# Performance work log

Hardware: AMD Instinct MI355X
Metric: run time of the kernel (lower is better)

The kernel has to match this reference:

```python
import jax, jax.numpy as jnp
import numpy as np
import math

B = 1048576          # number of query points
D = 3                # input_dim
L = 16               # num_levels
C = 2                # level_dim (features per level)
H = 16               # base_resolution
S = 1.0              # log2(per_level_scale)
LOG2_T = 19
MAX_PARAMS = 2 ** LOG2_T
HASH_ENTRIES = 524288
ALIGN = False        # align_corners
PRIMES = (1, 2654435761, 805459861)  # tcnn spatial hash primes


def _make_offsets():
    offs = [0]
    off = 0
    for l in range(L):
        res = int(np.ceil(H * (2.0 ** (S * l))))
        n = min(MAX_PARAMS, (res if ALIGN else res + 1) ** D)
        n = int(np.ceil(n / 8) * 8)
        off += n
        offs.append(off)
    return offs

OFFSETS = _make_offsets()
N_TABLE = OFFSETS[-1]  # 7131240
# 2^D corner offsets, corner i has bit d = (i >> d) & 1
_CORNERS = np.array([[(i >> d) & 1 for d in range(D)] for i in range(2 ** D)], dtype=np.uint32)


def _grid_encode(x01, table):
    """x01: [B, D] coords in [0, 1]; table: [N_TABLE, C]. Returns [B, L*C]."""
    corners_u = jnp.asarray(_CORNERS)                  # [8, D] uint32
    corners_b = jnp.asarray(_CORNERS.astype(bool))     # [8, D]
    outs = []
    for l in range(L):
        scale = (2.0 ** (S * l)) * H - 1.0
        res = int(math.ceil(scale)) + 1
        side = res if ALIGN else res + 1               # per-dim stride base
        hm = OFFSETS[l + 1] - OFFSETS[l]               # hashmap size of this level
        pos = x01 * jnp.float32(scale) + jnp.float32(0.0 if ALIGN else 0.5)
        pg = jnp.floor(pos)
        frac = pos - pg                                # [B, D]
        cg = pg.astype(jnp.uint32)[:, None, :] + corners_u[None]  # [B, 8, D]
        # trilinear weights: prod of frac (corner bit 1) or 1-frac (bit 0)
        w = jnp.prod(jnp.where(corners_b[None], frac[:, None, :], 1.0 - frac[:, None, :]), axis=-1)  # [B, 8]
        if side ** D <= hm:
            # dense (non-hashed) stride indexing
            strides = jnp.asarray(np.array([side ** d for d in range(D)], dtype=np.uint32))
            idx = jnp.sum(cg * strides[None, None, :], axis=-1, dtype=jnp.uint32) % jnp.uint32(hm)
        else:
            # spatial hash: xor of coord * prime, wrapping uint32 arithmetic
            h = cg[..., 0] * jnp.uint32(PRIMES[0])
            for d in range(1, D):
                h = h ^ (cg[..., d] * jnp.uint32(PRIMES[d]))
            idx = h % jnp.uint32(hm)
        feats = table[(idx + jnp.uint32(OFFSETS[l])).astype(jnp.int32)]   # [B, 8, C] gather
        outs.append(jnp.sum(w[..., None] * feats, axis=1))                # [B, C]
    # matches outputs.permute(1,0,2).reshape(B, L*C): level features concatenated per point
    return jnp.concatenate(outs, axis=-1)


def setup_inputs():
    key = jax.random.key(0)
    k1, k2, k3 = jax.random.split(key, 3)
    inputs = jax.random.uniform(k1, (B, D), dtype=jnp.float32, minval=-1.0, maxval=1.0)
    ext_embeddings = jax.random.uniform(k2, (HASH_ENTRIES, C), dtype=jnp.float32, minval=-1e-4, maxval=1e-4)
    own_embeddings = jax.random.uniform(k3, (N_TABLE - HASH_ENTRIES, C), dtype=jnp.float32, minval=-1e-4, maxval=1e-4)
    return {"inputs": inputs, "ext_embeddings": ext_embeddings, "own_embeddings": own_embeddings}


def reference(inputs, ext_embeddings, own_embeddings):
    bound = 1.0
    table = jnp.concatenate([ext_embeddings, own_embeddings], axis=0)  # [N_TABLE, C]
    x01 = (inputs + bound) / (2.0 * bound)
    return _grid_encode(x01, table)
```

## Files before the change

### kernel.cpp

```cpp
#include <hip/hip_runtime.h>
#include <hip/hip_cooperative_groups.h>
#include <stdint.h>

namespace cg = cooperative_groups;


constexpr uint32_t OFF[16] = {
    0u, 4920u, 40864u, 315496u, 839784u, 1364072u, 1888360u, 2412648u,
    2936936u, 3461224u, 3985512u, 4509800u, 5034088u, 5558376u, 6082664u, 6606952u
};

#define HASH_ENTRIES 524288u
#define HASH_MASK    (HASH_ENTRIES - 1u)
#define P1 2654435761u
#define P2 805459861u

typedef float floatx2 __attribute__((ext_vector_type(2)));
typedef float floatx4 __attribute__((ext_vector_type(4)));

template<int L>
__device__ __forceinline__ void do_level(
    float x01, float y01, float z01,
    const float2* __restrict__ ext, const float2* __restrict__ own,
    float* __restrict__ ws, int B, int p)
{
    constexpr float scale = (float)((16u << L) - 1u);
    const float px = x01 * scale + 0.5f;
    const float py = y01 * scale + 0.5f;
    const float pz = z01 * scale + 0.5f;
    const float fxf = floorf(px), fyf = floorf(py), fzf = floorf(pz);
    const float tx = px - fxf, ty = py - fyf, tz = pz - fzf;
    const uint32_t x0 = (uint32_t)(int)fxf;
    const uint32_t y0 = (uint32_t)(int)fyf;
    const uint32_t z0 = (uint32_t)(int)fzf;

    float2 f[8];
    if constexpr (L < 3) {
        constexpr uint32_t side = (16u << L) + 1u;
        constexpr uint32_t s2 = side * side;
        const uint32_t base = OFF[L] + x0 + y0 * side + z0 * s2;
#pragma unroll
        for (int i = 0; i < 8; ++i) {
            f[i] = ext[base + (uint32_t)(i & 1)
                           + (uint32_t)((i >> 1) & 1) * side
                           + (uint32_t)((i >> 2) & 1) * s2];
        }
    } else {
        const uint32_t hx0 = x0,       hx1 = x0 + 1u;
        const uint32_t hy0 = y0 * P1,  hy1 = (y0 + 1u) * P1;
        const uint32_t hz0 = z0 * P2,  hz1 = (z0 + 1u) * P2;
#pragma unroll
        for (int i = 0; i < 8; ++i) {
            const uint32_t gi = (((i & 1) ? hx1 : hx0) ^
                                 ((i & 2) ? hy1 : hy0) ^
                                 ((i & 4) ? hz1 : hz0)) & HASH_MASK;
            if constexpr (L == 3) {
                const uint32_t gg = gi + OFF[3];
                const float2* q = (gg < HASH_ENTRIES)
                                    ? (ext + gg)
                                    : (own + (gg - HASH_ENTRIES));
                f[i] = *q;
            } else {
                f[i] = own[(OFF[L] - HASH_ENTRIES) + gi];
            }
        }
    }

    float r0 = 0.0f, r1 = 0.0f;
#pragma unroll
    for (int i = 0; i < 8; ++i) {
        const float wi = ((i & 1) ? tx : 1.0f - tx)
                       * ((i & 2) ? ty : 1.0f - ty)
                       * ((i & 4) ? tz : 1.0f - tz);
        r0 += wi * f[i].x;
        r1 += wi * f[i].y;
    }
    floatx2 v = { r0, r1 };
    __builtin_nontemporal_store(v, (floatx2*)(ws + (size_t)L * 2 * B + 2 * p));
}

__global__ __launch_bounds__(256, 4) void coop_kernel(
    const float* __restrict__ xyz,
    const float2* __restrict__ ext,
    const float2* __restrict__ own,
    float* __restrict__ ws,
    float* __restrict__ out,
    int B)
{
    cg::grid_group grid = cg::this_grid();
    const int NT  = (int)(gridDim.x * 256u);
    const int tid = (int)(blockIdx.x * 256u + threadIdx.x);

    float cx[4], cy[4], cz[4];
#pragma unroll
    for (int i = 0; i < 4; ++i) {
        const int p = tid + i * NT;
        if (p < B) {
            cx[i] = (__builtin_nontemporal_load(&xyz[3 * p + 0]) + 1.0f) * 0.5f;
            cy[i] = (__builtin_nontemporal_load(&xyz[3 * p + 1]) + 1.0f) * 0.5f;
            cz[i] = (__builtin_nontemporal_load(&xyz[3 * p + 2]) + 1.0f) * 0.5f;
        } else {
            cx[i] = cy[i] = cz[i] = 0.0f;
        }
    }

#define LEVEL_STEP(L)                                                        \
    {                                                                        \
        _Pragma("unroll")                                                    \
        for (int i = 0; i < 4; ++i) {                                        \
            const int p = tid + i * NT;                                      \
            if (p < B) do_level<L>(cx[i], cy[i], cz[i], ext, own, ws, B, p); \
        }                                                                    \
        grid.sync();                                                         \
    }

    LEVEL_STEP(0)  LEVEL_STEP(1)  LEVEL_STEP(2)  LEVEL_STEP(3)
    LEVEL_STEP(4)  LEVEL_STEP(5)  LEVEL_STEP(6)  LEVEL_STEP(7)
    LEVEL_STEP(8)  LEVEL_STEP(9)  LEVEL_STEP(10) LEVEL_STEP(11)
    LEVEL_STEP(12) LEVEL_STEP(13) LEVEL_STEP(14) LEVEL_STEP(15)
#undef LEVEL_STEP

#pragma unroll
    for (int i = 0; i < 4; ++i) {
        const int p = tid + i * NT;
        if (p >= B) continue;
        float v[32];
#pragma unroll
        for (int l = 0; l < 16; ++l) {
            floatx2 t = *(const floatx2*)(ws + (size_t)l * 2 * B + 2 * p);
            v[2 * l + 0] = t.x;
            v[2 * l + 1] = t.y;
        }
        floatx4* o4 = (floatx4*)(out + (size_t)p * 32);
#pragma unroll
        for (int k = 0; k < 8; ++k) {
            floatx4 q = { v[4 * k + 0], v[4 * k + 1],
                          v[4 * k + 2], v[4 * k + 3] };
            o4[k] = q;
        }
    }
}

template<int L, bool DIRECT>
__global__ __launch_bounds__(256) void phase_kernel(
    const float* __restrict__ xyz,
    const float2* __restrict__ ext,
    const float2* __restrict__ own,
    float* __restrict__ dst,
    int B)
{
    const int b = blockIdx.x * 256 + threadIdx.x;
    if (b >= B) return;
    const float x01 = (__builtin_nontemporal_load(&xyz[3 * b + 0]) + 1.0f) * 0.5f;
    const float y01 = (__builtin_nontemporal_load(&xyz[3 * b + 1]) + 1.0f) * 0.5f;
    const float z01 = (__builtin_nontemporal_load(&xyz[3 * b + 2]) + 1.0f) * 0.5f;
    if constexpr (DIRECT) {
        constexpr float scale = (float)((16u << L) - 1u);
        const float px = x01 * scale + 0.5f;
        const float py = y01 * scale + 0.5f;
        const float pz = z01 * scale + 0.5f;
        const float fxf = floorf(px), fyf = floorf(py), fzf = floorf(pz);
        const float tx = px - fxf, ty = py - fyf, tz = pz - fzf;
        const uint32_t x0 = (uint32_t)(int)fxf;
        const uint32_t y0 = (uint32_t)(int)fyf;
        const uint32_t z0 = (uint32_t)(int)fzf;
        float2 f[8];
        if constexpr (L < 3) {
            constexpr uint32_t side = (16u << L) + 1u;
            constexpr uint32_t s2 = side * side;
            const uint32_t base = OFF[L] + x0 + y0 * side + z0 * s2;
#pragma unroll
            for (int i = 0; i < 8; ++i)
                f[i] = ext[base + (uint32_t)(i & 1)
                               + (uint32_t)((i >> 1) & 1) * side
                               + (uint32_t)((i >> 2) & 1) * s2];
        } else {
            const uint32_t hx0 = x0,       hx1 = x0 + 1u;
            const uint32_t hy0 = y0 * P1,  hy1 = (y0 + 1u) * P1;
            const uint32_t hz0 = z0 * P2,  hz1 = (z0 + 1u) * P2;
#pragma unroll
            for (int i = 0; i < 8; ++i) {
                const uint32_t gi = (((i & 1) ? hx1 : hx0) ^
                                     ((i & 2) ? hy1 : hy0) ^
                                     ((i & 4) ? hz1 : hz0)) & HASH_MASK;
                if constexpr (L == 3) {
                    const uint32_t gg = gi + OFF[3];
                    const float2* q = (gg < HASH_ENTRIES)
                                        ? (ext + gg)
                                        : (own + (gg - HASH_ENTRIES));
                    f[i] = *q;
                } else {
                    f[i] = own[(OFF[L] - HASH_ENTRIES) + gi];
                }
            }
        }
        float r0 = 0.0f, r1 = 0.0f;
#pragma unroll
        for (int i = 0; i < 8; ++i) {
            const float wi = ((i & 1) ? tx : 1.0f - tx)
                           * ((i & 2) ? ty : 1.0f - ty)
                           * ((i & 4) ? tz : 1.0f - tz);
            r0 += wi * f[i].x;
            r1 += wi * f[i].y;
        }
        floatx2 v = { r0, r1 };
        *(floatx2*)(dst + (size_t)b * 32 + 2 * L) = v;
    } else {
        do_level<L>(x01, y01, z01, ext, own, dst, B, b);
    }
}

__global__ __launch_bounds__(256) void transpose_kernel(
    const float* __restrict__ ws, float* __restrict__ out, int B)
{
    const int b = blockIdx.x * 256 + threadIdx.x;
    if (b >= B) return;
    float v[32];
#pragma unroll
    for (int l = 0; l < 16; ++l) {
        floatx2 t = *(const floatx2*)(ws + (size_t)l * 2 * B + 2 * b);
        v[2 * l + 0] = t.x;
        v[2 * l + 1] = t.y;
    }
    floatx4* o4 = (floatx4*)(out + (size_t)b * 32);
#pragma unroll
    for (int k = 0; k < 8; ++k) {
        floatx4 q = { v[4 * k + 0], v[4 * k + 1], v[4 * k + 2], v[4 * k + 3] };
        o4[k] = q;
    }
}

template<bool DIRECT>
static inline void launch_phases(const float* xyz, const float2* ext,
                                 const float2* own, float* dst, int B,
                                 int grid, hipStream_t stream) {
    phase_kernel< 0, DIRECT><<<grid, 256, 0, stream>>>(xyz, ext, own, dst, B);
    phase_kernel< 1, DIRECT><<<grid, 256, 0, stream>>>(xyz, ext, own, dst, B);
    phase_kernel< 2, DIRECT><<<grid, 256, 0, stream>>>(xyz, ext, own, dst, B);
    phase_kernel< 3, DIRECT><<<grid, 256, 0, stream>>>(xyz, ext, own, dst, B);
    phase_kernel< 4, DIRECT><<<grid, 256, 0, stream>>>(xyz, ext, own, dst, B);
    phase_kernel< 5, DIRECT><<<grid, 256, 0, stream>>>(xyz, ext, own, dst, B);
    phase_kernel< 6, DIRECT><<<grid, 256, 0, stream>>>(xyz, ext, own, dst, B);
    phase_kernel< 7, DIRECT><<<grid, 256, 0, stream>>>(xyz, ext, own, dst, B);
    phase_kernel< 8, DIRECT><<<grid, 256, 0, stream>>>(xyz, ext, own, dst, B);
    phase_kernel< 9, DIRECT><<<grid, 256, 0, stream>>>(xyz, ext, own, dst, B);
    phase_kernel<10, DIRECT><<<grid, 256, 0, stream>>>(xyz, ext, own, dst, B);
    phase_kernel<11, DIRECT><<<grid, 256, 0, stream>>>(xyz, ext, own, dst, B);
    phase_kernel<12, DIRECT><<<grid, 256, 0, stream>>>(xyz, ext, own, dst, B);
    phase_kernel<13, DIRECT><<<grid, 256, 0, stream>>>(xyz, ext, own, dst, B);
    phase_kernel<14, DIRECT><<<grid, 256, 0, stream>>>(xyz, ext, own, dst, B);
    phase_kernel<15, DIRECT><<<grid, 256, 0, stream>>>(xyz, ext, own, dst, B);
}

extern "C" void kernel_launch(void* const* d_in, const int* in_sizes, int n_in,
                              void* d_out, int out_size, void* d_ws, size_t ws_size,
                              hipStream_t stream) {
    const float*  xyz = (const float*)d_in[0];
    const float2* ext = (const float2*)d_in[1];
    const float2* own = (const float2*)d_in[2];
    float* out = (float*)d_out;
    const int B = in_sizes[0] / 3;
    const int grid = (B + 255) / 256;
    const size_t need = (size_t)B * 32 * sizeof(float);

    int dev = 0;
    hipGetDevice(&dev);
    int cus = 0;
    hipDeviceGetAttribute(&cus, hipDeviceAttributeMultiprocessorCount, dev);
    int occ = 0;
    hipOccupancyMaxActiveBlocksPerMultiprocessor(&occ, coop_kernel, 256, 0);
    const int gridNeeded = (B + 4 * 256 - 1) / (4 * 256);

    if (ws_size >= need && occ > 0 && (long)occ * cus >= gridNeeded) {
        float* ws = (float*)d_ws;
        int Bv = B;
        void* args[6];
        args[0] = (void*)&xyz; args[1] = (void*)&ext; args[2] = (void*)&own;
        args[3] = (void*)&ws;  args[4] = (void*)&out; args[5] = (void*)&Bv;
        hipLaunchCooperativeKernel((const void*)coop_kernel,
                                   dim3(gridNeeded), dim3(256), args, 0, stream);
    } else if (ws_size >= need) {
        float* ws = (float*)d_ws;
        launch_phases<false>(xyz, ext, own, ws, B, grid, stream);
        transpose_kernel<<<grid, 256, 0, stream>>>(ws, out, B);
    } else {
        launch_phases<true>(xyz, ext, own, out, B, grid, stream);
    }
}
```

Baseline: 662.8 us.

## Batch hash gathers across points, fuse dense levels into final pass, double occupancy

The cooperative kernel now handles 2 points per thread instead of 4 and raises launch bounds to 8 blocks per CU. Each hash level computes all corner indices for both points first, then issues all 16 gathers, so more loads are in flight. The three dense levels, whose tables are small and cache-resident, are computed directly in the final output pass, which removes three grid syncs and shrinks the workspace to 26 floats per point. The risks are higher register pressure from the batched gathers under the tighter register budget, and a larger grid that must still fit co-resident for the cooperative launch.

```diff
diff --git a/kernel.cpp b/kernel.cpp
--- a/kernel.cpp
+++ b/kernel.cpp
@@ -14,16 +14,83 @@
 #define HASH_MASK    (HASH_ENTRIES - 1u)
 #define P1 2654435761u
 #define P2 805459861u
+#define PPT 2
 
 typedef float floatx2 __attribute__((ext_vector_type(2)));
 typedef float floatx4 __attribute__((ext_vector_type(4)));
 
 template<int L>
-__device__ __forceinline__ void do_level(
-    float x01, float y01, float z01,
+__device__ __forceinline__ void hash_phase(
+    const float* cx, const float* cy, const float* cz,
     const float2* __restrict__ ext, const float2* __restrict__ own,
-    float* __restrict__ ws, int B, int p)
+    float* __restrict__ ws, int B, int tid, int NT)
 {
+    static_assert(L >= 3, "hash levels only");
+    uint32_t gi[PPT][8];
+    float txa[PPT], tya[PPT], tza[PPT];
+#pragma unroll
+    for (int i = 0; i < PPT; ++i) {
+        constexpr float scale = (float)((16u << L) - 1u);
+        const float px = cx[i] * scale + 0.5f;
+        const float py = cy[i] * scale + 0.5f;
+        const float pz = cz[i] * scale + 0.5f;
+        const float fxf = floorf(px), fyf = floorf(py), fzf = floorf(pz);
+        txa[i] = px - fxf; tya[i] = py - fyf; tza[i] = pz - fzf;
+        const uint32_t x0 = (uint32_t)(int)fxf;
+        const uint32_t y0 = (uint32_t)(int)fyf;
+        const uint32_t z0 = (uint32_t)(int)fzf;
+        const uint32_t hx0 = x0,       hx1 = x0 + 1u;
+        const uint32_t hy0 = y0 * P1,  hy1 = (y0 + 1u) * P1;
+        const uint32_t hz0 = z0 * P2,  hz1 = (z0 + 1u) * P2;
+#pragma unroll
+        for (int c = 0; c < 8; ++c) {
+            gi[i][c] = (((c & 1) ? hx1 : hx0) ^
+                        ((c & 2) ? hy1 : hy0) ^
+                        ((c & 4) ? hz1 : hz0)) & HASH_MASK;
+        }
+    }
+
+    float2 f[PPT][8];
+#pragma unroll
+    for (int i = 0; i < PPT; ++i) {
+#pragma unroll
+        for (int c = 0; c < 8; ++c) {
+            if constexpr (L == 3) {
+                const uint32_t gg = gi[i][c] + OFF[3];
+                const float2* q = (gg < HASH_ENTRIES)
+                                    ? (ext + gg)
+                                    : (own + (gg - HASH_ENTRIES));
+                f[i][c] = *q;
+            } else {
+                f[i][c] = own[(OFF[L] - HASH_ENTRIES) + gi[i][c]];
+            }
+        }
+    }
+
+#pragma unroll
+    for (int i = 0; i < PPT; ++i) {
+        const int p = tid + i * NT;
+        if (p >= B) continue;
+        float r0 = 0.0f, r1 = 0.0f;
+#pragma unroll
+        for (int c = 0; c < 8; ++c) {
+            const float wi = ((c & 1) ? txa[i] : 1.0f - txa[i])
+                           * ((c & 2) ? tya[i] : 1.0f - tya[i])
+                           * ((c & 4) ? tza[i] : 1.0f - tza[i]);
+            r0 += wi * f[i][c].x;
+            r1 += wi * f[i][c].y;
+        }
+        floatx2 v = { r0, r1 };
+        __builtin_nontemporal_store(v,
+            (floatx2*)(ws + (size_t)(L - 3) * 2 * B + 2 * p));
+    }
+}
+
+template<int L>
+__device__ __forceinline__ float2 dense_level(
+    float x01, float y01, float z01, const float2* __restrict__ ext)
+{
+    static_assert(L < 3, "dense levels only");
     constexpr float scale = (float)((16u << L) - 1u);
     const float px = x01 * scale + 0.5f;
     const float py = y01 * scale + 0.5f;
@@ -33,18 +100,125 @@
     const uint32_t x0 = (uint32_t)(int)fxf;
     const uint32_t y0 = (uint32_t)(int)fyf;
     const uint32_t z0 = (uint32_t)(int)fzf;
-
+    constexpr uint32_t side = (16u << L) + 1u;
+    constexpr uint32_t s2 = side * side;
+    const uint32_t base = OFF[L] + x0 + y0 * side + z0 * s2;
+    float r0 = 0.0f, r1 = 0.0f;
+#pragma unroll
+    for (int c = 0; c < 8; ++c) {
+        const float2 f = ext[base + (uint32_t)(c & 1)
+                                  + (uint32_t)((c >> 1) & 1) * side
+                                  + (uint32_t)((c >> 2) & 1) * s2];
+        const float wi = ((c & 1) ? tx : 1.0f - tx)
+                       * ((c & 2) ? ty : 1.0f - ty)
+                       * ((c & 4) ? tz : 1.0f - tz);
+        r0 += wi * f.x;
+        r1 += wi * f.y;
+    }
+    return make_float2(r0, r1);
+}
+
+__global__ __launch_bounds__(256, 8) void coop_kernel(
+    const float* __restrict__ xyz,
+    const float2* __restrict__ ext,
+    const float2* __restrict__ own,
+    float* __restrict__ ws,
+    float* __restrict__ out,
+    int B)
+{
+    cg::grid_group grid = cg::this_grid();
+    const int NT  = (int)(gridDim.x * 256u);
+    const int tid = (int)(blockIdx.x * 256u + threadIdx.x);
+
+    float cx[PPT], cy[PPT], cz[PPT];
+#pragma unroll
+    for (int i = 0; i < PPT; ++i) {
+        const int p = tid + i * NT;
+        if (p < B) {
+            cx[i] = (__builtin_nontemporal_load(&xyz[3 * p + 0]) + 1.0f) * 0.5f;
+            cy[i] = (__builtin_nontemporal_load(&xyz[3 * p + 1]) + 1.0f) * 0.5f;
+            cz[i] = (__builtin_nontemporal_load(&xyz[3 * p + 2]) + 1.0f) * 0.5f;
+        } else {
+            cx[i] = cy[i] = cz[i] = 0.0f;
+        }
+    }
+
+#define HP(L) hash_phase<L>(cx, cy, cz, ext, own, ws, B, tid, NT)
+    HP(3);  grid.sync();
+    HP(4);  grid.sync();
+    HP(5);  grid.sync();
+    HP(6);  grid.sync();
+    HP(7);  grid.sync();
+    HP(8);  grid.sync();
+    HP(9);  grid.sync();
+    HP(10); grid.sync();
+    HP(11); grid.sync();
+    HP(12); grid.sync();
+    HP(13); grid.sync();
+    HP(14); grid.sync();
+    HP(15);
+#undef HP
+
+#pragma unroll
+    for (int i = 0; i < PPT; ++i) {
+        const int p = tid + i * NT;
+        if (p >= B) continue;
+        float v[32];
+        const float2 d0 = dense_level<0>(cx[i], cy[i], cz[i], ext);
+        const float2 d1 = dense_level<1>(cx[i], cy[i], cz[i], ext);
+        const float2 d2 = dense_level<2>(cx[i], cy[i], cz[i], ext);
+        v[0] = d0.x; v[1] = d0.y;
+        v[2] = d1.x; v[3] = d1.y;
+        v[4] = d2.x; v[5] = d2.y;
+#pragma unroll
+        for (int l = 3; l < 16; ++l) {
+            floatx2 t = __builtin_nontemporal_load(
+                (const floatx2*)(ws + (size_t)(l - 3) * 2 * B + 2 * p));
+            v[2 * l + 0] = t.x;
+            v[2 * l + 1] = t.y;
+        }
+        floatx4* o4 = (floatx4*)(out + (size_t)p * 32);
+#pragma unroll
+        for (int k = 0; k < 8; ++k) {
+            floatx4 q = { v[4 * k + 0], v[4 * k + 1],
+                          v[4 * k + 2], v[4 * k + 3] };
+            o4[k] = q;
+        }
+    }
+}
+
+template<int L>
+__global__ __launch_bounds__(256) void phase_kernel(
+    const float* __restrict__ xyz,
+    const float2* __restrict__ ext,
+    const float2* __restrict__ own,
+    float* __restrict__ dst,
+    int B)
+{
+    const int b = blockIdx.x * 256 + threadIdx.x;
+    if (b >= B) return;
+    const float x01 = (__builtin_nontemporal_load(&xyz[3 * b + 0]) + 1.0f) * 0.5f;
+    const float y01 = (__builtin_nontemporal_load(&xyz[3 * b + 1]) + 1.0f) * 0.5f;
+    const float z01 = (__builtin_nontemporal_load(&xyz[3 * b + 2]) + 1.0f) * 0.5f;
+    constexpr float scale = (float)((16u << L) - 1u);
+    const float px = x01 * scale + 0.5f;
+    const float py = y01 * scale + 0.5f;
+    const float pz = z01 * scale + 0.5f;
+    const float fxf = floorf(px), fyf = floorf(py), fzf = floorf(pz);
+    const float tx = px - fxf, ty = py - fyf, tz = pz - fzf;
+    const uint32_t x0 = (uint32_t)(int)fxf;
+    const uint32_t y0 = (uint32_t)(int)fyf;
+    const uint32_t z0 = (uint32_t)(int)fzf;
     float2 f[8];
     if constexpr (L < 3) {
         constexpr uint32_t side = (16u << L) + 1u;
         constexpr uint32_t s2 = side * side;
         const uint32_t base = OFF[L] + x0 + y0 * side + z0 * s2;
 #pragma unroll
-        for (int i = 0; i < 8; ++i) {
+        for (int i = 0; i < 8; ++i)
             f[i] = ext[base + (uint32_t)(i & 1)
                            + (uint32_t)((i >> 1) & 1) * side
                            + (uint32_t)((i >> 2) & 1) * s2];
-        }
     } else {
         const uint32_t hx0 = x0,       hx1 = x0 + 1u;
         const uint32_t hy0 = y0 * P1,  hy1 = (y0 + 1u) * P1;
@@ -65,7 +239,6 @@
             }
         }
     }
-
     float r0 = 0.0f, r1 = 0.0f;
 #pragma unroll
     for (int i = 0; i < 8; ++i) {
@@ -76,180 +249,28 @@
         r1 += wi * f[i].y;
     }
     floatx2 v = { r0, r1 };
-    __builtin_nontemporal_store(v, (floatx2*)(ws + (size_t)L * 2 * B + 2 * p));
-}
-
-__global__ __launch_bounds__(256, 4) void coop_kernel(
-    const float* __restrict__ xyz,
-    const float2* __restrict__ ext,
-    const float2* __restrict__ own,
-    float* __restrict__ ws,
-    float* __restrict__ out,
-    int B)
-{
-    cg::grid_group grid = cg::this_grid();
-    const int NT  = (int)(gridDim.x * 256u);
-    const int tid = (int)(blockIdx.x * 256u + threadIdx.x);
-
-    float cx[4], cy[4], cz[4];
-#pragma unroll
-    for (int i = 0; i < 4; ++i) {
-        const int p = tid + i * NT;
-        if (p < B) {
-            cx[i] = (__builtin_nontemporal_load(&xyz[3 * p + 0]) + 1.0f) * 0.5f;
-            cy[i] = (__builtin_nontemporal_load(&xyz[3 * p + 1]) + 1.0f) * 0.5f;
-            cz[i] = (__builtin_nontemporal_load(&xyz[3 * p + 2]) + 1.0f) * 0.5f;
-        } else {
-            cx[i] = cy[i] = cz[i] = 0.0f;
-        }
-    }
-
-#define LEVEL_STEP(L)                                                        \
-    {                                                                        \
-        _Pragma("unroll")                                                    \
-        for (int i = 0; i < 4; ++i) {                                        \
-            const int p = tid + i * NT;                                      \
-            if (p < B) do_level<L>(cx[i], cy[i], cz[i], ext, own, ws, B, p); \
-        }                                                                    \
-        grid.sync();                                                         \
-    }
-
-    LEVEL_STEP(0)  LEVEL_STEP(1)  LEVEL_STEP(2)  LEVEL_STEP(3)
-    LEVEL_STEP(4)  LEVEL_STEP(5)  LEVEL_STEP(6)  LEVEL_STEP(7)
-    LEVEL_STEP(8)  LEVEL_STEP(9)  LEVEL_STEP(10) LEVEL_STEP(11)
-    LEVEL_STEP(12) LEVEL_STEP(13) LEVEL_STEP(14) LEVEL_STEP(15)
-#undef LEVEL_STEP
-
-#pragma unroll
-    for (int i = 0; i < 4; ++i) {
-        const int p = tid + i * NT;
-        if (p >= B) continue;
-        float v[32];
-#pragma unroll
-        for (int l = 0; l < 16; ++l) {
-            floatx2 t = *(const floatx2*)(ws + (size_t)l * 2 * B + 2 * p);
-            v[2 * l + 0] = t.x;
-            v[2 * l + 1] = t.y;
-        }
-        floatx4* o4 = (floatx4*)(out + (size_t)p * 32);
-#pragma unroll
-        for (int k = 0; k < 8; ++k) {
-            floatx4 q = { v[4 * k + 0], v[4 * k + 1],
-                          v[4 * k + 2], v[4 * k + 3] };
-            o4[k] = q;
-        }
-    }
-}
-
-template<int L, bool DIRECT>
-__global__ __launch_bounds__(256) void phase_kernel(
-    const float* __restrict__ xyz,
-    const float2* __restrict__ ext,
-    const float2* __restrict__ own,
-    float* __restrict__ dst,
-    int B)
-{
-    const int b = blockIdx.x * 256 + threadIdx.x;
-    if (b >= B) return;
-    const float x01 = (__builtin_nontemporal_load(&xyz[3 * b + 0]) + 1.0f) * 0.5f;
-    const float y01 = (__builtin_nontemporal_load(&xyz[3 * b + 1]) + 1.0f) * 0.5f;
-    const float z01 = (__builtin_nontemporal_load(&xyz[3 * b + 2]) + 1.0f) * 0.5f;
-    if constexpr (DIRECT) {
-        constexpr float scale = (float)((16u << L) - 1u);
-        const float px = x01 * scale + 0.5f;
-        const float py = y01 * scale + 0.5f;
-        const float pz = z01 * scale + 0.5f;
-        const float fxf = floorf(px), fyf = floorf(py), fzf = floorf(pz);
-        const float tx = px - fxf, ty = py - fyf, tz = pz - fzf;
-        const uint32_t x0 = (uint32_t)(int)fxf;
-        const uint32_t y0 = (uint32_t)(int)fyf;
-        const uint32_t z0 = (uint32_t)(int)fzf;
-        float2 f[8];
-        if constexpr (L < 3) {
-            constexpr uint32_t side = (16u << L) + 1u;
-            constexpr uint32_t s2 = side * side;
-            const uint32_t base = OFF[L] + x0 + y0 * side + z0 * s2;
-#pragma unroll
-            for (int i = 0; i < 8; ++i)
-                f[i] = ext[base + (uint32_t)(i & 1)
-                               + (uint32_t)((i >> 1) & 1) * side
-                               + (uint32_t)((i >> 2) & 1) * s2];
-        } else {
-            const uint32_t hx0 = x0,       hx1 = x0 + 1u;
-            const uint32_t hy0 = y0 * P1,  hy1 = (y0 + 1u) * P1;
-            const uint32_t hz0 = z0 * P2,  hz1 = (z0 + 1u) * P2;
-#pragma unroll
-            for (int i = 0; i < 8; ++i) {
-                const uint32_t gi = (((i & 1) ? hx1 : hx0) ^
-                                     ((i & 2) ? hy1 : hy0) ^
-                                     ((i & 4) ? hz1 : hz0)) & HASH_MASK;
-                if constexpr (L == 3) {
-                    const uint32_t gg = gi + OFF[3];
-                    const float2* q = (gg < HASH_ENTRIES)
-                                        ? (ext + gg)
-                                        : (own + (gg - HASH_ENTRIES));
-                    f[i] = *q;
-                } else {
-                    f[i] = own[(OFF[L] - HASH_ENTRIES) + gi];
-                }
-            }
-        }
-        float r0 = 0.0f, r1 = 0.0f;
-#pragma unroll
-        for (int i = 0; i < 8; ++i) {
-            const float wi = ((i & 1) ? tx : 1.0f - tx)
-                           * ((i & 2) ? ty : 1.0f - ty)
-                           * ((i & 4) ? tz : 1.0f - tz);
-            r0 += wi * f[i].x;
-            r1 += wi * f[i].y;
-        }
-        floatx2 v = { r0, r1 };
-        *(floatx2*)(dst + (size_t)b * 32 + 2 * L) = v;
-    } else {
-        do_level<L>(x01, y01, z01, ext, own, dst, B, b);
-    }
-}
-
-__global__ __launch_bounds__(256) void transpose_kernel(
-    const float* __restrict__ ws, float* __restrict__ out, int B)
-{
-    const int b = blockIdx.x * 256 + threadIdx.x;
-    if (b >= B) return;
-    float v[32];
-#pragma unroll
-    for (int l = 0; l < 16; ++l) {
-        floatx2 t = *(const floatx2*)(ws + (size_t)l * 2 * B + 2 * b);
-        v[2 * l + 0] = t.x;
-        v[2 * l + 1] = t.y;
-    }
-    floatx4* o4 = (floatx4*)(out + (size_t)b * 32);
-#pragma unroll
-    for (int k = 0; k < 8; ++k) {
-        floatx4 q = { v[4 * k + 0], v[4 * k + 1], v[4 * k + 2], v[4 * k + 3] };
-        o4[k] = q;
-    }
-}
-
-template<bool DIRECT>
-static inline void launch_phases(const float* xyz, const float2* ext,
-                                 const float2* own, float* dst, int B,
-                                 int grid, hipStream_t stream) {
-    phase_kernel< 0, DIRECT><<<grid, 256, 0, stream>>>(xyz, ext, own, dst, B);
-    phase_kernel< 1, DIRECT><<<grid, 256, 0, stream>>>(xyz, ext, own, dst, B);
-    phase_kernel< 2, DIRECT><<<grid, 256, 0, stream>>>(xyz, ext, own, dst, B);
-    phase_kernel< 3, DIRECT><<<grid, 256, 0, stream>>>(xyz, ext, own, dst, B);
-    phase_kernel< 4, DIRECT><<<grid, 256, 0, stream>>>(xyz, ext, own, dst, B);
-    phase_kernel< 5, DIRECT><<<grid, 256, 0, stream>>>(xyz, ext, own, dst, B);
-    phase_kernel< 6, DIRECT><<<grid, 256, 0, stream>>>(xyz, ext, own, dst, B);
-    phase_kernel< 7, DIRECT><<<grid, 256, 0, stream>>>(xyz, ext, own, dst, B);
-    phase_kernel< 8, DIRECT><<<grid, 256, 0, stream>>>(xyz, ext, own, dst, B);
-    phase_kernel< 9, DIRECT><<<grid, 256, 0, stream>>>(xyz, ext, own, dst, B);
-    phase_kernel<10, DIRECT><<<grid, 256, 0, stream>>>(xyz, ext, own, dst, B);
-    phase_kernel<11, DIRECT><<<grid, 256, 0, stream>>>(xyz, ext, own, dst, B);
-    phase_kernel<12, DIRECT><<<grid, 256, 0, stream>>>(xyz, ext, own, dst, B);
-    phase_kernel<13, DIRECT><<<grid, 256, 0, stream>>>(xyz, ext, own, dst, B);
-    phase_kernel<14, DIRECT><<<grid, 256, 0, stream>>>(xyz, ext, own, dst, B);
-    phase_kernel<15, DIRECT><<<grid, 256, 0, stream>>>(xyz, ext, own, dst, B);
+    *(floatx2*)(dst + (size_t)b * 32 + 2 * L) = v;
+}
+
+static inline void launch_fallback(const float* xyz, const float2* ext,
+                                   const float2* own, float* dst, int B,
+                                   int grid, hipStream_t stream) {
+    phase_kernel< 0><<<grid, 256, 0, stream>>>(xyz, ext, own, dst, B);
+    phase_kernel< 1><<<grid, 256, 0, stream>>>(xyz, ext, own, dst, B);
+    phase_kernel< 2><<<grid, 256, 0, stream>>>(xyz, ext, own, dst, B);
+    phase_kernel< 3><<<grid, 256, 0, stream>>>(xyz, ext, own, dst, B);
+    phase_kernel< 4><<<grid, 256, 0, stream>>>(xyz, ext, own, dst, B);
+    phase_kernel< 5><<<grid, 256, 0, stream>>>(xyz, ext, own, dst, B);
+    phase_kernel< 6><<<grid, 256, 0, stream>>>(xyz, ext, own, dst, B);
+    phase_kernel< 7><<<grid, 256, 0, stream>>>(xyz, ext, own, dst, B);
+    phase_kernel< 8><<<grid, 256, 0, stream>>>(xyz, ext, own, dst, B);
+    phase_kernel< 9><<<grid, 256, 0, stream>>>(xyz, ext, own, dst, B);
+    phase_kernel<10><<<grid, 256, 0, stream>>>(xyz, ext, own, dst, B);
+    phase_kernel<11><<<grid, 256, 0, stream>>>(xyz, ext, own, dst, B);
+    phase_kernel<12><<<grid, 256, 0, stream>>>(xyz, ext, own, dst, B);
+    phase_kernel<13><<<grid, 256, 0, stream>>>(xyz, ext, own, dst, B);
+    phase_kernel<14><<<grid, 256, 0, stream>>>(xyz, ext, own, dst, B);
+    phase_kernel<15><<<grid, 256, 0, stream>>>(xyz, ext, own, dst, B);
 }
 
 extern "C" void kernel_launch(void* const* d_in, const int* in_sizes, int n_in,
@@ -260,8 +281,7 @@
     const float2* own = (const float2*)d_in[2];
     float* out = (float*)d_out;
     const int B = in_sizes[0] / 3;
-    const int grid = (B + 255) / 256;
-    const size_t need = (size_t)B * 32 * sizeof(float);
+    const size_t need = (size_t)B * 26 * sizeof(float);
 
     int dev = 0;
     hipGetDevice(&dev);
@@ -269,7 +289,7 @@
     hipDeviceGetAttribute(&cus, hipDeviceAttributeMultiprocessorCount, dev);
     int occ = 0;
     hipOccupancyMaxActiveBlocksPerMultiprocessor(&occ, coop_kernel, 256, 0);
-    const int gridNeeded = (B + 4 * 256 - 1) / (4 * 256);
+    const int gridNeeded = (B + PPT * 256 - 1) / (PPT * 256);
 
     if (ws_size >= need && occ > 0 && (long)occ * cus >= gridNeeded) {
         float* ws = (float*)d_ws;
@@ -279,11 +299,8 @@
         args[3] = (void*)&ws;  args[4] = (void*)&out; args[5] = (void*)&Bv;
         hipLaunchCooperativeKernel((const void*)coop_kernel,
                                    dim3(gridNeeded), dim3(256), args, 0, stream);
-    } else if (ws_size >= need) {
-        float* ws = (float*)d_ws;
-        launch_phases<false>(xyz, ext, own, ws, B, grid, stream);
-        transpose_kernel<<<grid, 256, 0, stream>>>(ws, out, B);
     } else {
-        launch_phases<true>(xyz, ext, own, out, B, grid, stream);
-    }
-}
+        const int grid = (B + 255) / 256;
+        launch_fallback(xyz, ext, own, out, B, grid, stream);
+    }
+}
```

After: 884.7 us. +33.5%, slower.
